# Performance work log

Hardware: AMD Instinct MI355X
Metric: run time of the kernel (lower is better)

Reference implementation:

```python
import jax, jax.numpy as jnp
import numpy as np

N_VERTICES = 2000
N_SENSORY = 784
N_EDGES = 500_000
BATCH = 32
T_STEPS = 5
LR_VALUES = 0.1


def setup_inputs() -> dict:
    key = jax.random.key(0)
    k1, k2, k3 = jax.random.split(key, 3)
    values = jax.random.normal(k1, (BATCH, N_VERTICES), dtype=jnp.float32)
    # weight_init 'normal 0.0' -> std = max(0.01, 0) = 0.01 in the torch module
    weights = jax.random.normal(k2, (N_EDGES,), dtype=jnp.float32) * 0.01
    edge_index = jax.random.randint(k3, (2, N_EDGES), 0, N_VERTICES, dtype=jnp.int32)
    # sensory nodes (first 784) are clamped; only internal nodes update
    update_mask = jnp.arange(N_VERTICES) >= N_SENSORY  # bool [N]
    return {
        "values": values,
        "weights": weights,
        "edge_index": edge_index,
        "update_mask": update_mask,
        "T": T_STEPS,
    }


def reference(values, weights, edge_index, update_mask, T):
    """Iterative predictive-coding message passing.

    Each step:
      pred_i  = sum_{e: dst(e)=i} w_e * f(values[src(e)])   (gather-mul-scatter)
      err     = values - pred
      back_j  = sum_{e: src(e)=j} w_e * err[dst(e)]          (reverse scatter)
      dv      = err - f'(values) * back                      (dE/dx)
      values  = values - lr * dv   (sensory nodes clamped)
    """
    src, dst = edge_index[0], edge_index[1]
    n = values.shape[1]
    mask = update_mask[None, :]

    def step(v, _):
        fx = jnp.tanh(v)                                   # [B, N]
        msg = weights[None, :] * fx[:, src]                # [B, E]
        pred = jax.ops.segment_sum(msg.T, dst, num_segments=n).T  # [B, N]
        err = v - pred                                     # [B, N]
        w_err = weights[None, :] * err[:, dst]             # [B, E]
        back = jax.ops.segment_sum(w_err.T, src, num_segments=n).T  # [B, N]
        fprime = 1.0 - fx * fx                             # tanh'
        dv = err - fprime * back
        v_new = jnp.where(mask, v - LR_VALUES * dv, v)
        return v_new, None

    v_final, _ = jax.lax.scan(step, values, None, length=T)
    return v_final
```

## Files before the change

### kernel.cpp

```cpp
#include <hip/hip_runtime.h>
#include <hip/hip_bf16.h>


#define N_V     2000
#define N_SENS  784
#define N_INT   (N_V - N_SENS)
#define N_E     500000
#define T_STEPS 5
#define LR_VAL  0.1f
#define NVB     (N_V * 32)
#define NVH     (N_V * 16)
#define KP      2016
#define NCH     63
#define NT1     125
#define NT2     76
#define FRAG_N  (2 * NCH * 64 * 8)
#define NBLK    250
#define EPB     2000

typedef float  f32x4 __attribute__((ext_vector_type(4)));
typedef short  s16x8 __attribute__((ext_vector_type(8)));

__device__ __forceinline__ float bits_to_f32(unsigned u) {
    union { unsigned u; float f; } c; c.u = u; return c.f;
}
__device__ __forceinline__ unsigned f32_to_bits(float f) {
    union { float f; unsigned u; } c; c.f = f; return c.u;
}
__device__ __forceinline__ unsigned short f32_to_bf16(float f) {
    unsigned u = f32_to_bits(f);
    return (unsigned short)((u + 0x7FFFu + ((u >> 16) & 1u)) >> 16);
}
__device__ __forceinline__ float bf16_to_f32(unsigned short s) {
    return bits_to_f32((unsigned)s << 16);
}

__device__ __forceinline__ int aposKB(int k, int b) {
    int c = k >> 5, q = (k >> 3) & 3, j = k & 7;
    int h = b >> 4, m = b & 15;
    return (((h * NCH + c) * 64) + q * 16 + m) * 8 + j;
}


__global__ void k_zero_u4(uint4* p, int n4) {
    uint4 z = {0u, 0u, 0u, 0u};
    for (int t = blockIdx.x * blockDim.x + threadIdx.x; t < n4; t += gridDim.x * blockDim.x)
        p[t] = z;
}

__global__ __launch_bounds__(256) void k_cnt(const int* __restrict__ dst,
                                             int* __restrict__ cnt_g) {
    __shared__ int cnt[NT1];
    int b = blockIdx.x;
    for (int i = threadIdx.x; i < NT1; i += 256) cnt[i] = 0;
    __syncthreads();
    int base = b * EPB;
    for (int e = base + threadIdx.x; e < base + EPB; e += 256)
        atomicAdd(&cnt[dst[e] >> 4], 1);
    __syncthreads();
    for (int t = threadIdx.x; t < NT1; t += 256)
        cnt_g[t * 256 + b] = cnt[t];
}

__global__ __launch_bounds__(256) void k_scan_a(const int* __restrict__ cnt_g,
                                                int* __restrict__ base_g,
                                                int* __restrict__ totals) {
    __shared__ int sh[256];
    int t = blockIdx.x, tid = threadIdx.x;
    int v = (tid < NBLK) ? cnt_g[t * 256 + tid] : 0;
    sh[tid] = v;
    __syncthreads();
    for (int off = 1; off < 256; off <<= 1) {
        int x = (tid >= off) ? sh[tid - off] : 0;
        __syncthreads();
        sh[tid] += x;
        __syncthreads();
    }
    if (tid < NBLK) base_g[t * 256 + tid] = sh[tid] - v;
    if (tid == 255) totals[t] = sh[255];
}

__global__ void k_scan_b(const int* __restrict__ totals, int* __restrict__ tile_start) {
    if (threadIdx.x == 0 && blockIdx.x == 0) {
        int acc = 0;
        for (int t = 0; t < NT1; ++t) { tile_start[t] = acc; acc += totals[t]; }
        tile_start[NT1] = acc;
    }
}

__global__ __launch_bounds__(256) void k_place(
        const int* __restrict__ src, const int* __restrict__ dst,
        const float* __restrict__ w, const int* __restrict__ base_g,
        const int* __restrict__ tile_start, unsigned* __restrict__ pk_g) {
    __shared__ int cur[NT1];
    int b = blockIdx.x;
    for (int t = threadIdx.x; t < NT1; t += 256)
        cur[t] = tile_start[t] + base_g[t * 256 + b];
    __syncthreads();
    int base = b * EPB;
    for (int e = base + threadIdx.x; e < base + EPB; e += 256) {
        int d = dst[e];
        int tb = d >> 4;
        unsigned pk = ((unsigned)f32_to_bf16(w[e]) << 16)
                    | ((unsigned)(d & 15) << 11) | (unsigned)src[e];
        int p = atomicAdd(&cur[tb], 1);
        pk_g[p] = pk;
    }
}

__global__ __launch_bounds__(256) void k_build(
        const unsigned* __restrict__ pk_g, const int* __restrict__ tile_start,
        uint4* __restrict__ WAbf4, unsigned short* __restrict__ WAd) {
    __shared__ float acc[8][KP];
    int tile = blockIdx.x >> 1, half = blockIdx.x & 1;
    for (int i = threadIdx.x; i < 8 * KP / 4; i += 256)
        ((float4*)&acc[0][0])[i] = make_float4(0.f, 0.f, 0.f, 0.f);
    __syncthreads();
    int beg = tile_start[tile], end = tile_start[tile + 1];
    for (int e = beg + threadIdx.x; e < end; e += 256) {
        unsigned pk = pk_g[e];
        int row = (int)((pk >> 11) & 15u);
        if ((row >> 3) == half)
            atomicAdd(&acc[row & 7][pk & 0x7FFu], bf16_to_f32((unsigned short)(pk >> 16)));
    }
    __syncthreads();
    for (int i = threadIdx.x; i < 8 * 252; i += 256) {
        int rr = i / 252, g = i - rr * 252;
        int c = g >> 2, q = g & 3;
        int col = g * 8;
        unsigned short r[8];
        #pragma unroll
        for (int j = 0; j < 8; ++j) r[j] = f32_to_bf16(acc[rr][col + j]);
        uint4 val = *(const uint4*)r;
        int m = half * 8 + rr;
        WAbf4[((tile * NCH + c) * 64) + q * 16 + m] = val;
        *(uint4*)(WAd + (size_t)(tile * 16 + m) * KP + col) = val;
    }
}

__global__ void k_trB(const unsigned short* __restrict__ WAd, uint4* __restrict__ WBf4) {
    int t = blockIdx.x * blockDim.x + threadIdx.x;
    if (t < NT2 * NCH * 64) {
        int tile = t / (NCH * 64);
        int rem = t - tile * (NCH * 64);
        int c = rem >> 6, l = rem & 63;
        int jcol = N_SENS + tile * 16 + (l & 15);
        int k0 = c * 32 + (l >> 4) * 8;
        unsigned short r[8];
        #pragma unroll
        for (int j = 0; j < 8; ++j)
            r[j] = (k0 + j < N_V) ? WAd[(size_t)(k0 + j) * KP + jcol] : (unsigned short)0;
        WBf4[t] = *(const uint4*)r;
    }
}

__global__ void k_init(const float* __restrict__ vin, float* __restrict__ v,
                       unsigned short* __restrict__ fxA) {
    int t = blockIdx.x * blockDim.x + threadIdx.x;
    if (t < NVB) {
        int i = t >> 5, b = t & 31;
        float x = vin[b * N_V + i];
        v[t] = x;
        fxA[aposKB(i, b)] = f32_to_bf16(tanhf(x));
    }
}

__global__ __launch_bounds__(256) void k_gemm1(
        const uint4* __restrict__ WAbf4, const uint4* __restrict__ fxA4,
        const float* __restrict__ v_cur, unsigned short* __restrict__ errA) {
    __shared__ float red[2304];
    int tile = blockIdx.x;
    int w = threadIdx.x >> 6, l = threadIdx.x & 63;
    int cbeg = w * 16, cend = (cbeg + 16 < NCH) ? cbeg + 16 : NCH;
    f32x4 acc0 = {0.f, 0.f, 0.f, 0.f}, acc1 = {0.f, 0.f, 0.f, 0.f};
    for (int c = cbeg; c < cend; ++c) {
        uint4 bfrag = WAbf4[(tile * NCH + c) * 64 + l];
        uint4 a0 = fxA4[c * 64 + l];
        uint4 a1 = fxA4[(NCH + c) * 64 + l];
        acc0 = __builtin_amdgcn_mfma_f32_16x16x32_bf16(*(s16x8*)&a0, *(s16x8*)&bfrag, acc0, 0, 0, 0);
        acc1 = __builtin_amdgcn_mfma_f32_16x16x32_bf16(*(s16x8*)&a1, *(s16x8*)&bfrag, acc1, 0, 0, 0);
    }
    float* my = &red[w * 576 + l * 9];
    #pragma unroll
    for (int r = 0; r < 4; ++r) { my[r] = acc0[r]; my[4 + r] = acc1[r]; }
    __syncthreads();
    if (w == 0) {
        float s[8];
        #pragma unroll
        for (int r = 0; r < 8; ++r)
            s[r] = red[l * 9 + r] + red[576 + l * 9 + r]
                 + red[1152 + l * 9 + r] + red[1728 + l * 9 + r];
        int i = tile * 16 + (l & 15);
        int q = l >> 4;
        int c2 = i >> 5, q2 = (i >> 3) & 3, j2 = i & 7;
        #pragma unroll
        for (int h = 0; h < 2; ++h) {
            const float4 v4 = *(const float4*)(v_cur + (i << 5) + h * 16 + q * 4);
            int base = ((h * NCH + c2) * 64 + q2 * 16) * 8 + j2;
            errA[base + (q * 4 + 0) * 8] = f32_to_bf16(v4.x - s[h * 4 + 0]);
            errA[base + (q * 4 + 1) * 8] = f32_to_bf16(v4.y - s[h * 4 + 1]);
            errA[base + (q * 4 + 2) * 8] = f32_to_bf16(v4.z - s[h * 4 + 2]);
            errA[base + (q * 4 + 3) * 8] = f32_to_bf16(v4.w - s[h * 4 + 3]);
        }
    }
}

__global__ __launch_bounds__(256) void k_gemm2(
        const uint4* __restrict__ WBf4, const uint4* __restrict__ errA4,
        unsigned short* __restrict__ errA, unsigned short* __restrict__ fxA,
        float* __restrict__ v_cur) {
    __shared__ float red[2304];
    int tile = blockIdx.x;
    int w = threadIdx.x >> 6, l = threadIdx.x & 63;
    int cbeg = w * 16, cend = (cbeg + 16 < NCH) ? cbeg + 16 : NCH;
    f32x4 acc0 = {0.f, 0.f, 0.f, 0.f}, acc1 = {0.f, 0.f, 0.f, 0.f};
    for (int c = cbeg; c < cend; ++c) {
        uint4 bfrag = WBf4[(tile * NCH + c) * 64 + l];
        uint4 a0 = errA4[c * 64 + l];
        uint4 a1 = errA4[(NCH + c) * 64 + l];
        acc0 = __builtin_amdgcn_mfma_f32_16x16x32_bf16(*(s16x8*)&a0, *(s16x8*)&bfrag, acc0, 0, 0, 0);
        acc1 = __builtin_amdgcn_mfma_f32_16x16x32_bf16(*(s16x8*)&a1, *(s16x8*)&bfrag, acc1, 0, 0, 0);
    }
    float* my = &red[w * 576 + l * 9];
    #pragma unroll
    for (int r = 0; r < 4; ++r) { my[r] = acc0[r]; my[4 + r] = acc1[r]; }
    __syncthreads();
    if (w == 0) {
        float s[8];
        #pragma unroll
        for (int r = 0; r < 8; ++r)
            s[r] = red[l * 9 + r] + red[576 + l * 9 + r]
                 + red[1152 + l * 9 + r] + red[1728 + l * 9 + r];
        int j = N_SENS + tile * 16 + (l & 15);
        int q = l >> 4;
        int c2 = j >> 5, q2 = (j >> 3) & 3, j2 = j & 7;
        #pragma unroll
        for (int h = 0; h < 2; ++h) {
            float4 v4 = *(const float4*)(v_cur + (j << 5) + h * 16 + q * 4);
            int base = ((h * NCH + c2) * 64 + q2 * 16) * 8 + j2;
            float vv[4] = {v4.x, v4.y, v4.z, v4.w};
            #pragma unroll
            for (int r = 0; r < 4; ++r) {
                float back = s[h * 4 + r];
                float e0 = bf16_to_f32(errA[base + (q * 4 + r) * 8]);
                float fxv = tanhf(vv[r]);
                float vn = vv[r] - LR_VAL * (e0 - (1.f - fxv * fxv) * back);
                vv[r] = vn;
                fxA[base + (q * 4 + r) * 8] = f32_to_bf16(tanhf(vn));
            }
            float4 o = {vv[0], vv[1], vv[2], vv[3]};
            *(float4*)(v_cur + (j << 5) + h * 16 + q * 4) = o;
        }
    }
}

__global__ void k_out(const float* __restrict__ v, float* __restrict__ out) {
    int t = blockIdx.x * blockDim.x + threadIdx.x;
    if (t < NVB) {
        int b = t / N_V;
        int i = t - b * N_V;
        out[t] = v[(i << 5) + b];
    }
}

__global__ void k_cast_in(const float* __restrict__ vin, float* __restrict__ v) {
    int t = blockIdx.x * blockDim.x + threadIdx.x;
    if (t < NVB) {
        int i = t >> 5, b = t & 31;
        v[t] = vin[b * N_V + i];
    }
}


__global__ void k_zero_i32(int* a, int n) {
    int t = blockIdx.x * blockDim.x + threadIdx.x;
    if (t < n) a[t] = 0;
}

__global__ void k_hist(const int* __restrict__ src, const int* __restrict__ dst,
                       int* cnt_dst, int* cnt_src) {
    int e = blockIdx.x * blockDim.x + threadIdx.x;
    if (e < N_E) {
        atomicAdd(&cnt_dst[dst[e]], 1);
        atomicAdd(&cnt_src[src[e]], 1);
    }
}

__global__ __launch_bounds__(1024) void k_scan(int* cnt_a, int* rp_a,
                                               int* cnt_b, int* rp_b) {
    __shared__ int sh[1024];
    int t = threadIdx.x;
    for (int pass = 0; pass < 2; ++pass) {
        int* cnt = pass ? cnt_b : cnt_a;
        int* rp  = pass ? rp_b  : rp_a;
        int i0 = 2 * t, i1 = 2 * t + 1;
        int c0 = (i0 < N_V) ? cnt[i0] : 0;
        int c1 = (i1 < N_V) ? cnt[i1] : 0;
        __syncthreads();
        sh[t] = c0 + c1;
        __syncthreads();
        for (int off = 1; off < 1024; off <<= 1) {
            int v = (t >= off) ? sh[t - off] : 0;
            __syncthreads();
            sh[t] += v;
            __syncthreads();
        }
        int incl = sh[t];
        int e0 = incl - (c0 + c1);
        int e1 = e0 + c0;
        if (i0 <= N_V) rp[i0] = e0;
        if (i1 <= N_V) rp[i1] = e1;
        if (i0 < N_V) cnt[i0] = e0;
        if (i1 < N_V) cnt[i1] = e1;
    }
}

__global__ void k_scatter(const int* __restrict__ src, const int* __restrict__ dst,
                          const float* __restrict__ w,
                          int* cur_dst, int* cur_src,
                          unsigned* __restrict__ pk_dst, unsigned* __restrict__ pk_src) {
    int e = blockIdx.x * blockDim.x + threadIdx.x;
    if (e < N_E) {
        int s = src[e], d = dst[e];
        unsigned wbits = (unsigned)f32_to_bf16(w[e]);
        int p = atomicAdd(&cur_dst[d], 1);
        pk_dst[p] = (wbits << 16) | (unsigned)s;
        int q = atomicAdd(&cur_src[s], 1);
        pk_src[q] = (wbits << 16) | (unsigned)d;
    }
}

__global__ void k_fx_csr(const float* __restrict__ v, unsigned short* __restrict__ fx) {
    int t = blockIdx.x * blockDim.x + threadIdx.x;
    if (t < NVB) {
        int i = t >> 5, b = t & 31;
        int h = b >> 4, b16 = b & 15;
        fx[h * NVH + i * 16 + b16] = f32_to_bf16(tanhf(v[t]));
    }
}

__global__ __launch_bounds__(256) void k_pred_err(
        const float* __restrict__ v, const unsigned short* __restrict__ fx,
        const int* __restrict__ rp, const unsigned* __restrict__ pk,
        unsigned short* __restrict__ err) {
    __shared__ unsigned short tab[NVH];
    int h  = blockIdx.x / 250;
    int vg = blockIdx.x % 250;
    {
        const uint4* g = (const uint4*)(fx + h * NVH);
        uint4* l = (uint4*)tab;
        for (int i = threadIdx.x; i < NVH / 8; i += 256) l[i] = g[i];
    }
    __syncthreads();
    int wave = threadIdx.x >> 6;
    int lane = threadIdx.x & 63;
    int b16 = lane & 15, epar = lane >> 4;
    for (int k = 0; k < 2; ++k) {
        int vid = vg * 8 + wave * 2 + k;
        int beg = rp[vid], end = rp[vid + 1];
        float sum = 0.f;
        for (int e = beg + epar; e < end; e += 4) {
            unsigned p = pk[e];
            float w = bits_to_f32(p & 0xFFFF0000u);
            int nb = (int)(p & 0xFFFFu);
            sum += w * bf16_to_f32(tab[nb * 16 + b16]);
        }
        sum += __shfl_xor(sum, 16, 64);
        sum += __shfl_xor(sum, 32, 64);
        if (epar == 0) {
            float vo = v[(vid << 5) + h * 16 + b16];
            err[h * NVH + vid * 16 + b16] = f32_to_bf16(vo - sum);
        }
    }
}

__global__ __launch_bounds__(256) void k_back_upd(
        const unsigned short* __restrict__ fx, const unsigned short* __restrict__ err,
        const int* __restrict__ rp, const unsigned* __restrict__ pk,
        float* __restrict__ v) {
    __shared__ unsigned short tab[NVH];
    int h  = blockIdx.x / 152;
    int vg = blockIdx.x % 152;
    {
        const uint4* g = (const uint4*)(err + h * NVH);
        uint4* l = (uint4*)tab;
        for (int i = threadIdx.x; i < NVH / 8; i += 256) l[i] = g[i];
    }
    __syncthreads();
    int wave = threadIdx.x >> 6;
    int lane = threadIdx.x & 63;
    int b16 = lane & 15, epar = lane >> 4;
    for (int k = 0; k < 2; ++k) {
        int vid = N_SENS + vg * 8 + wave * 2 + k;
        if (vid >= N_V) continue;
        int beg = rp[vid], end = rp[vid + 1];
        float sum = 0.f;
        for (int e = beg + epar; e < end; e += 4) {
            unsigned p = pk[e];
            float w = bits_to_f32(p & 0xFFFF0000u);
            int nb = (int)(p & 0xFFFFu);
            sum += w * bf16_to_f32(tab[nb * 16 + b16]);
        }
        sum += __shfl_xor(sum, 16, 64);
        sum += __shfl_xor(sum, 32, 64);
        if (epar == 0) {
            float e0  = bf16_to_f32(tab[vid * 16 + b16]);
            float fxv = bf16_to_f32(fx[h * NVH + vid * 16 + b16]);
            float dv = e0 - (1.f - fxv * fxv) * sum;
            v[(vid << 5) + h * 16 + b16] -= LR_VAL * dv;
        }
    }
}


extern "C" void kernel_launch(void* const* d_in, const int* in_sizes, int n_in,
                              void* d_out, int out_size, void* d_ws, size_t ws_size,
                              hipStream_t stream) {
    const float* vals = (const float*)d_in[0];
    const float* wts  = (const float*)d_in[1];
    const int* ei = (const int*)d_in[2];
    const int* src = ei;
    const int* dst = ei + N_E;
    float* out = (float*)d_out;

    const int EB = (N_E + 255) / 256;

    const size_t WABF_T = (size_t)NT1 * NCH * 64;
    const size_t WBF_T  = (size_t)NT2 * NCH * 64;
    const size_t WAD_N  = (size_t)N_V * KP;
    const size_t need = (size_t)N_E * 4 + 2 * NT1 * 256 * 4 + 512 * 4
                      + WAD_N * 2 + WABF_T * 16 + WBF_T * 16
                      + 2 * (size_t)FRAG_N * 2 + NVB * 4 + 256;

    if (ws_size >= need) {
        unsigned* pk_g = (unsigned*)d_ws;
        int* cnt_g  = (int*)(pk_g + N_E);
        int* base_g = cnt_g + NT1 * 256;
        int* totals = base_g + NT1 * 256;
        int* tile_start = totals + 128;
        unsigned short* WAd = (unsigned short*)(tile_start + 384);
        uint4* WAbf4 = (uint4*)(WAd + WAD_N);
        uint4* WBf4  = WAbf4 + WABF_T;
        unsigned short* fxA  = (unsigned short*)(WBf4 + WBF_T);
        unsigned short* errA = fxA + FRAG_N;
        float* v_cur = (float*)(errA + FRAG_N);

        k_zero_u4<<<64, 256, 0, stream>>>((uint4*)fxA, (int)(2 * (size_t)FRAG_N * 2 / 16));
        k_cnt<<<NBLK, 256, 0, stream>>>(dst, cnt_g);
        k_scan_a<<<NT1, 256, 0, stream>>>(cnt_g, base_g, totals);
        k_scan_b<<<1, 64, 0, stream>>>(totals, tile_start);
        k_place<<<NBLK, 256, 0, stream>>>(src, dst, wts, base_g, tile_start, pk_g);
        k_build<<<2 * NT1, 256, 0, stream>>>(pk_g, tile_start, WAbf4, WAd);
        k_trB<<<(int)((WBF_T + 255) / 256), 256, 0, stream>>>(WAd, WBf4);
        k_init<<<250, 256, 0, stream>>>(vals, v_cur, fxA);

        for (int t = 0; t < T_STEPS; ++t) {
            k_gemm1<<<NT1, 256, 0, stream>>>(WAbf4, (const uint4*)fxA, v_cur, errA);
            k_gemm2<<<NT2, 256, 0, stream>>>(WBf4, (const uint4*)errA, errA, fxA, v_cur);
        }
        k_out<<<250, 256, 0, stream>>>(v_cur, out);
    } else {
        float* v_cur = (float*)d_ws;
        unsigned short* fx_g  = (unsigned short*)(v_cur + NVB);
        unsigned short* err_g = fx_g + NVB;
        int* rp_dst  = (int*)(err_g + NVB);
        int* rp_src  = rp_dst + 2048;
        int* cur_dst = rp_src + 2048;
        int* cur_src = cur_dst + 2048;
        unsigned* pk_dst = (unsigned*)(cur_src + 2048);
        unsigned* pk_src = pk_dst + N_E;

        k_zero_i32<<<16, 256, 0, stream>>>(cur_dst, 4096);
        k_hist<<<EB, 256, 0, stream>>>(src, dst, cur_dst, cur_src);
        k_scan<<<1, 1024, 0, stream>>>(cur_dst, rp_dst, cur_src, rp_src);
        k_scatter<<<EB, 256, 0, stream>>>(src, dst, wts, cur_dst, cur_src,
                                          pk_dst, pk_src);
        k_cast_in<<<250, 256, 0, stream>>>(vals, v_cur);
        for (int t = 0; t < T_STEPS; ++t) {
            k_fx_csr<<<250, 256, 0, stream>>>(v_cur, fx_g);
            k_pred_err<<<500, 256, 0, stream>>>(v_cur, fx_g, rp_dst, pk_dst, err_g);
            k_back_upd<<<304, 256, 0, stream>>>(fx_g, err_g, rp_src, pk_src, v_cur);
        }
        k_out<<<250, 256, 0, stream>>>(v_cur, out);
    }
}
```

Before: 180.1 us.

## Fuse setup and time-step kernels into two cooperative persistent kernels

Replaces the chain of about eighteen small kernel launches (build passes, init, ten GEMM launches, output) with two cooperative kernels that use grid-wide syncs between phases. The step kernel also splits each GEMM tile across two blocks by batch half, so 250 blocks each run one MFMA chain instead of 125/76 blocks running two. Only the 16 padding rows of the fragment buffers are zeroed now, not the whole buffers. The aim is to cut launch gaps and raise occupancy, at the cost of grid.sync overhead and a dependence on all 250 blocks being co-resident.

New measurement: 612.8 us. 3.4x slower.

```diff
diff --git a/kernel.cpp b/kernel.cpp
--- a/kernel.cpp
+++ b/kernel.cpp
@@ -1,5 +1,6 @@
 #include <hip/hip_runtime.h>
 #include <hip/hip_bf16.h>
+#include <hip/hip_cooperative_groups.h>
 
 
 #define N_V     2000
@@ -18,6 +19,8 @@
 #define NBLK    250
 #define EPB     2000
 
+namespace cg = cooperative_groups;
+
 typedef float  f32x4 __attribute__((ext_vector_type(4)));
 typedef short  s16x8 __attribute__((ext_vector_type(8)));
 
@@ -42,232 +45,212 @@
 }
 
 
-__global__ void k_zero_u4(uint4* p, int n4) {
-    uint4 z = {0u, 0u, 0u, 0u};
-    for (int t = blockIdx.x * blockDim.x + threadIdx.x; t < n4; t += gridDim.x * blockDim.x)
-        p[t] = z;
-}
-
-__global__ __launch_bounds__(256) void k_cnt(const int* __restrict__ dst,
-                                             int* __restrict__ cnt_g) {
-    __shared__ int cnt[NT1];
-    int b = blockIdx.x;
-    for (int i = threadIdx.x; i < NT1; i += 256) cnt[i] = 0;
-    __syncthreads();
-    int base = b * EPB;
-    for (int e = base + threadIdx.x; e < base + EPB; e += 256)
-        atomicAdd(&cnt[dst[e] >> 4], 1);
-    __syncthreads();
-    for (int t = threadIdx.x; t < NT1; t += 256)
-        cnt_g[t * 256 + b] = cnt[t];
-}
-
-__global__ __launch_bounds__(256) void k_scan_a(const int* __restrict__ cnt_g,
-                                                int* __restrict__ base_g,
-                                                int* __restrict__ totals) {
-    __shared__ int sh[256];
-    int t = blockIdx.x, tid = threadIdx.x;
-    int v = (tid < NBLK) ? cnt_g[t * 256 + tid] : 0;
-    sh[tid] = v;
-    __syncthreads();
-    for (int off = 1; off < 256; off <<= 1) {
-        int x = (tid >= off) ? sh[tid - off] : 0;
-        __syncthreads();
-        sh[tid] += x;
-        __syncthreads();
-    }
-    if (tid < NBLK) base_g[t * 256 + tid] = sh[tid] - v;
-    if (tid == 255) totals[t] = sh[255];
-}
-
-__global__ void k_scan_b(const int* __restrict__ totals, int* __restrict__ tile_start) {
-    if (threadIdx.x == 0 && blockIdx.x == 0) {
-        int acc = 0;
-        for (int t = 0; t < NT1; ++t) { tile_start[t] = acc; acc += totals[t]; }
-        tile_start[NT1] = acc;
-    }
-}
-
-__global__ __launch_bounds__(256) void k_place(
+__global__ __launch_bounds__(256) void k_build_all(
         const int* __restrict__ src, const int* __restrict__ dst,
-        const float* __restrict__ w, const int* __restrict__ base_g,
-        const int* __restrict__ tile_start, unsigned* __restrict__ pk_g) {
-    __shared__ int cur[NT1];
-    int b = blockIdx.x;
-    for (int t = threadIdx.x; t < NT1; t += 256)
-        cur[t] = tile_start[t] + base_g[t * 256 + b];
-    __syncthreads();
-    int base = b * EPB;
-    for (int e = base + threadIdx.x; e < base + EPB; e += 256) {
-        int d = dst[e];
-        int tb = d >> 4;
-        unsigned pk = ((unsigned)f32_to_bf16(w[e]) << 16)
-                    | ((unsigned)(d & 15) << 11) | (unsigned)src[e];
-        int p = atomicAdd(&cur[tb], 1);
-        pk_g[p] = pk;
-    }
-}
-
-__global__ __launch_bounds__(256) void k_build(
-        const unsigned* __restrict__ pk_g, const int* __restrict__ tile_start,
-        uint4* __restrict__ WAbf4, unsigned short* __restrict__ WAd) {
+        const float* __restrict__ w, const float* __restrict__ vin,
+        int* cnt_g, int* base_g, int* totals, int* tile_start,
+        unsigned* pk_g, uint4* WAbf4, unsigned short* WAd, uint4* WBf4,
+        unsigned short* fxA, unsigned short* errA, float* v_cur) {
+    cg::grid_group grid = cg::this_grid();
     __shared__ float acc[8][KP];
-    int tile = blockIdx.x >> 1, half = blockIdx.x & 1;
-    for (int i = threadIdx.x; i < 8 * KP / 4; i += 256)
-        ((float4*)&acc[0][0])[i] = make_float4(0.f, 0.f, 0.f, 0.f);
-    __syncthreads();
-    int beg = tile_start[tile], end = tile_start[tile + 1];
-    for (int e = beg + threadIdx.x; e < end; e += 256) {
-        unsigned pk = pk_g[e];
-        int row = (int)((pk >> 11) & 15u);
-        if ((row >> 3) == half)
-            atomicAdd(&acc[row & 7][pk & 0x7FFu], bf16_to_f32((unsigned short)(pk >> 16)));
-    }
-    __syncthreads();
-    for (int i = threadIdx.x; i < 8 * 252; i += 256) {
-        int rr = i / 252, g = i - rr * 252;
-        int c = g >> 2, q = g & 3;
-        int col = g * 8;
-        unsigned short r[8];
-        #pragma unroll
-        for (int j = 0; j < 8; ++j) r[j] = f32_to_bf16(acc[rr][col + j]);
-        uint4 val = *(const uint4*)r;
-        int m = half * 8 + rr;
-        WAbf4[((tile * NCH + c) * 64) + q * 16 + m] = val;
-        *(uint4*)(WAd + (size_t)(tile * 16 + m) * KP + col) = val;
-    }
-}
-
-__global__ void k_trB(const unsigned short* __restrict__ WAd, uint4* __restrict__ WBf4) {
-    int t = blockIdx.x * blockDim.x + threadIdx.x;
-    if (t < NT2 * NCH * 64) {
-        int tile = t / (NCH * 64);
-        int rem = t - tile * (NCH * 64);
-        int c = rem >> 6, l = rem & 63;
-        int jcol = N_SENS + tile * 16 + (l & 15);
-        int k0 = c * 32 + (l >> 4) * 8;
-        unsigned short r[8];
-        #pragma unroll
-        for (int j = 0; j < 8; ++j)
-            r[j] = (k0 + j < N_V) ? WAd[(size_t)(k0 + j) * KP + jcol] : (unsigned short)0;
-        WBf4[t] = *(const uint4*)r;
-    }
-}
-
-__global__ void k_init(const float* __restrict__ vin, float* __restrict__ v,
-                       unsigned short* __restrict__ fxA) {
-    int t = blockIdx.x * blockDim.x + threadIdx.x;
-    if (t < NVB) {
-        int i = t >> 5, b = t & 31;
-        float x = vin[b * N_V + i];
-        v[t] = x;
-        fxA[aposKB(i, b)] = f32_to_bf16(tanhf(x));
-    }
-}
-
-__global__ __launch_bounds__(256) void k_gemm1(
-        const uint4* __restrict__ WAbf4, const uint4* __restrict__ fxA4,
-        const float* __restrict__ v_cur, unsigned short* __restrict__ errA) {
-    __shared__ float red[2304];
-    int tile = blockIdx.x;
-    int w = threadIdx.x >> 6, l = threadIdx.x & 63;
-    int cbeg = w * 16, cend = (cbeg + 16 < NCH) ? cbeg + 16 : NCH;
-    f32x4 acc0 = {0.f, 0.f, 0.f, 0.f}, acc1 = {0.f, 0.f, 0.f, 0.f};
-    for (int c = cbeg; c < cend; ++c) {
-        uint4 bfrag = WAbf4[(tile * NCH + c) * 64 + l];
-        uint4 a0 = fxA4[c * 64 + l];
-        uint4 a1 = fxA4[(NCH + c) * 64 + l];
-        acc0 = __builtin_amdgcn_mfma_f32_16x16x32_bf16(*(s16x8*)&a0, *(s16x8*)&bfrag, acc0, 0, 0, 0);
-        acc1 = __builtin_amdgcn_mfma_f32_16x16x32_bf16(*(s16x8*)&a1, *(s16x8*)&bfrag, acc1, 0, 0, 0);
-    }
-    float* my = &red[w * 576 + l * 9];
-    #pragma unroll
-    for (int r = 0; r < 4; ++r) { my[r] = acc0[r]; my[4 + r] = acc1[r]; }
-    __syncthreads();
-    if (w == 0) {
-        float s[8];
-        #pragma unroll
-        for (int r = 0; r < 8; ++r)
-            s[r] = red[l * 9 + r] + red[576 + l * 9 + r]
-                 + red[1152 + l * 9 + r] + red[1728 + l * 9 + r];
-        int i = tile * 16 + (l & 15);
-        int q = l >> 4;
-        int c2 = i >> 5, q2 = (i >> 3) & 3, j2 = i & 7;
-        #pragma unroll
-        for (int h = 0; h < 2; ++h) {
-            const float4 v4 = *(const float4*)(v_cur + (i << 5) + h * 16 + q * 4);
-            int base = ((h * NCH + c2) * 64 + q2 * 16) * 8 + j2;
-            errA[base + (q * 4 + 0) * 8] = f32_to_bf16(v4.x - s[h * 4 + 0]);
-            errA[base + (q * 4 + 1) * 8] = f32_to_bf16(v4.y - s[h * 4 + 1]);
-            errA[base + (q * 4 + 2) * 8] = f32_to_bf16(v4.z - s[h * 4 + 2]);
-            errA[base + (q * 4 + 3) * 8] = f32_to_bf16(v4.w - s[h * 4 + 3]);
-        }
-    }
-}
-
-__global__ __launch_bounds__(256) void k_gemm2(
-        const uint4* __restrict__ WBf4, const uint4* __restrict__ errA4,
-        unsigned short* __restrict__ errA, unsigned short* __restrict__ fxA,
-        float* __restrict__ v_cur) {
-    __shared__ float red[2304];
-    int tile = blockIdx.x;
-    int w = threadIdx.x >> 6, l = threadIdx.x & 63;
-    int cbeg = w * 16, cend = (cbeg + 16 < NCH) ? cbeg + 16 : NCH;
-    f32x4 acc0 = {0.f, 0.f, 0.f, 0.f}, acc1 = {0.f, 0.f, 0.f, 0.f};
-    for (int c = cbeg; c < cend; ++c) {
-        uint4 bfrag = WBf4[(tile * NCH + c) * 64 + l];
-        uint4 a0 = errA4[c * 64 + l];
-        uint4 a1 = errA4[(NCH + c) * 64 + l];
-        acc0 = __builtin_amdgcn_mfma_f32_16x16x32_bf16(*(s16x8*)&a0, *(s16x8*)&bfrag, acc0, 0, 0, 0);
-        acc1 = __builtin_amdgcn_mfma_f32_16x16x32_bf16(*(s16x8*)&a1, *(s16x8*)&bfrag, acc1, 0, 0, 0);
-    }
-    float* my = &red[w * 576 + l * 9];
-    #pragma unroll
-    for (int r = 0; r < 4; ++r) { my[r] = acc0[r]; my[4 + r] = acc1[r]; }
-    __syncthreads();
-    if (w == 0) {
-        float s[8];
-        #pragma unroll
-        for (int r = 0; r < 8; ++r)
-            s[r] = red[l * 9 + r] + red[576 + l * 9 + r]
-                 + red[1152 + l * 9 + r] + red[1728 + l * 9 + r];
-        int j = N_SENS + tile * 16 + (l & 15);
-        int q = l >> 4;
-        int c2 = j >> 5, q2 = (j >> 3) & 3, j2 = j & 7;
-        #pragma unroll
-        for (int h = 0; h < 2; ++h) {
-            float4 v4 = *(const float4*)(v_cur + (j << 5) + h * 16 + q * 4);
-            int base = ((h * NCH + c2) * 64 + q2 * 16) * 8 + j2;
-            float vv[4] = {v4.x, v4.y, v4.z, v4.w};
+    int bx = blockIdx.x, tid = threadIdx.x;
+
+    {
+        int t = bx * 256 + tid;
+        if (t < 16 * 32) {
+            int k = 2000 + (t >> 5), b = t & 31;
+            fxA[aposKB(k, b)] = 0;
+            errA[aposKB(k, b)] = 0;
+        }
+    }
+    {
+        int* cnt = (int*)&acc[0][0];
+        for (int i = tid; i < NT1; i += 256) cnt[i] = 0;
+        __syncthreads();
+        int base = bx * EPB;
+        for (int e = base + tid; e < base + EPB; e += 256)
+            atomicAdd(&cnt[dst[e] >> 4], 1);
+        __syncthreads();
+        for (int t = tid; t < NT1; t += 256) cnt_g[t * 256 + bx] = cnt[t];
+    }
+    grid.sync();
+    if (bx < NT1) {
+        int* sh = (int*)&acc[0][0];
+        int v = (tid < NBLK) ? cnt_g[bx * 256 + tid] : 0;
+        sh[tid] = v;
+        __syncthreads();
+        for (int off = 1; off < 256; off <<= 1) {
+            int x = (tid >= off) ? sh[tid - off] : 0;
+            __syncthreads();
+            sh[tid] += x;
+            __syncthreads();
+        }
+        if (tid < NBLK) base_g[bx * 256 + tid] = sh[tid] - v;
+        if (tid == 255) totals[bx] = sh[255];
+    }
+    grid.sync();
+    if (bx == 0 && tid == 0) {
+        int a = 0;
+        for (int t = 0; t < NT1; ++t) { tile_start[t] = a; a += totals[t]; }
+        tile_start[NT1] = a;
+    }
+    grid.sync();
+    {
+        int* cur = (int*)&acc[0][0];
+        for (int t = tid; t < NT1; t += 256)
+            cur[t] = tile_start[t] + base_g[t * 256 + bx];
+        __syncthreads();
+        int base = bx * EPB;
+        for (int e = base + tid; e < base + EPB; e += 256) {
+            int d = dst[e];
+            unsigned pk = ((unsigned)f32_to_bf16(w[e]) << 16)
+                        | ((unsigned)(d & 15) << 11) | (unsigned)src[e];
+            int p = atomicAdd(&cur[d >> 4], 1);
+            pk_g[p] = pk;
+        }
+    }
+    grid.sync();
+    {
+        int tile = bx >> 1, half = bx & 1;
+        for (int i = tid; i < 8 * KP / 4; i += 256)
+            ((float4*)&acc[0][0])[i] = make_float4(0.f, 0.f, 0.f, 0.f);
+        __syncthreads();
+        int beg = tile_start[tile], end = tile_start[tile + 1];
+        for (int e = beg + tid; e < end; e += 256) {
+            unsigned pk = pk_g[e];
+            int row = (int)((pk >> 11) & 15u);
+            if ((row >> 3) == half)
+                atomicAdd(&acc[row & 7][pk & 0x7FFu],
+                          bf16_to_f32((unsigned short)(pk >> 16)));
+        }
+        __syncthreads();
+        for (int i = tid; i < 8 * 252; i += 256) {
+            int rr = i / 252, gg = i - rr * 252;
+            int c = gg >> 2, q = gg & 3;
+            int col = gg * 8;
+            unsigned short r[8];
             #pragma unroll
-            for (int r = 0; r < 4; ++r) {
-                float back = s[h * 4 + r];
-                float e0 = bf16_to_f32(errA[base + (q * 4 + r) * 8]);
-                float fxv = tanhf(vv[r]);
-                float vn = vv[r] - LR_VAL * (e0 - (1.f - fxv * fxv) * back);
-                vv[r] = vn;
-                fxA[base + (q * 4 + r) * 8] = f32_to_bf16(tanhf(vn));
+            for (int j = 0; j < 8; ++j) r[j] = f32_to_bf16(acc[rr][col + j]);
+            uint4 val = *(const uint4*)r;
+            int m = half * 8 + rr;
+            WAbf4[((tile * NCH + c) * 64) + q * 16 + m] = val;
+            *(uint4*)(WAd + (size_t)(tile * 16 + m) * KP + col) = val;
+        }
+    }
+    grid.sync();
+    {
+        const int stride = NBLK * 256;
+        for (int t = bx * 256 + tid; t < NT2 * NCH * 64; t += stride) {
+            int tile = t / (NCH * 64);
+            int rem = t - tile * (NCH * 64);
+            int c = rem >> 6, l = rem & 63;
+            int jcol = N_SENS + tile * 16 + (l & 15);
+            int k0 = c * 32 + (l >> 4) * 8;
+            unsigned short r[8];
+            #pragma unroll
+            for (int j = 0; j < 8; ++j)
+                r[j] = (k0 + j < N_V) ? WAd[(size_t)(k0 + j) * KP + jcol]
+                                      : (unsigned short)0;
+            WBf4[t] = *(const uint4*)r;
+        }
+        for (int t = bx * 256 + tid; t < NVB; t += stride) {
+            int i = t >> 5, b = t & 31;
+            float x = vin[b * N_V + i];
+            v_cur[t] = x;
+            fxA[aposKB(i, b)] = f32_to_bf16(tanhf(x));
+        }
+    }
+}
+
+
+__global__ __launch_bounds__(256) void k_steps(
+        const uint4* __restrict__ WAbf4, const uint4* __restrict__ WBf4,
+        unsigned short* fxA, unsigned short* errA, float* v_cur,
+        float* __restrict__ out) {
+    cg::grid_group grid = cg::this_grid();
+    __shared__ float red[1300];
+    int bx = blockIdx.x, tid = threadIdx.x;
+    int w = tid >> 6, l = tid & 63;
+    const uint4* fxA4  = (const uint4*)fxA;
+    const uint4* errA4 = (const uint4*)errA;
+
+    for (int t = 0; t < T_STEPS; ++t) {
+        {
+            int tile = bx >> 1, h = bx & 1;
+            int cbeg = w * 16, cend = (cbeg + 16 < NCH) ? cbeg + 16 : NCH;
+            f32x4 acc = {0.f, 0.f, 0.f, 0.f};
+            for (int c = cbeg; c < cend; ++c) {
+                uint4 bfrag = WAbf4[(tile * NCH + c) * 64 + l];
+                uint4 a = fxA4[(h * NCH + c) * 64 + l];
+                acc = __builtin_amdgcn_mfma_f32_16x16x32_bf16(
+                          *(s16x8*)&a, *(s16x8*)&bfrag, acc, 0, 0, 0);
             }
-            float4 o = {vv[0], vv[1], vv[2], vv[3]};
-            *(float4*)(v_cur + (j << 5) + h * 16 + q * 4) = o;
-        }
-    }
-}
-
-__global__ void k_out(const float* __restrict__ v, float* __restrict__ out) {
-    int t = blockIdx.x * blockDim.x + threadIdx.x;
-    if (t < NVB) {
-        int b = t / N_V;
-        int i = t - b * N_V;
-        out[t] = v[(i << 5) + b];
-    }
-}
-
-__global__ void k_cast_in(const float* __restrict__ vin, float* __restrict__ v) {
-    int t = blockIdx.x * blockDim.x + threadIdx.x;
-    if (t < NVB) {
-        int i = t >> 5, b = t & 31;
-        v[t] = vin[b * N_V + i];
+            float* my = &red[w * 325 + l * 5];
+            #pragma unroll
+            for (int r = 0; r < 4; ++r) my[r] = acc[r];
+            __syncthreads();
+            if (w == 0) {
+                float s[4];
+                #pragma unroll
+                for (int r = 0; r < 4; ++r)
+                    s[r] = red[l * 5 + r] + red[325 + l * 5 + r]
+                         + red[650 + l * 5 + r] + red[975 + l * 5 + r];
+                int i = tile * 16 + (l & 15);
+                int q = l >> 4;
+                int c2 = i >> 5, q2 = (i >> 3) & 3, j2 = i & 7;
+                const float4 v4 = *(const float4*)(v_cur + (i << 5) + h * 16 + q * 4);
+                int base = ((h * NCH + c2) * 64 + q2 * 16) * 8 + j2;
+                errA[base + (q * 4 + 0) * 8] = f32_to_bf16(v4.x - s[0]);
+                errA[base + (q * 4 + 1) * 8] = f32_to_bf16(v4.y - s[1]);
+                errA[base + (q * 4 + 2) * 8] = f32_to_bf16(v4.z - s[2]);
+                errA[base + (q * 4 + 3) * 8] = f32_to_bf16(v4.w - s[3]);
+            }
+        }
+        grid.sync();
+        if (bx < 2 * NT2) {
+            int tile = bx >> 1, h = bx & 1;
+            int cbeg = w * 16, cend = (cbeg + 16 < NCH) ? cbeg + 16 : NCH;
+            f32x4 acc = {0.f, 0.f, 0.f, 0.f};
+            for (int c = cbeg; c < cend; ++c) {
+                uint4 bfrag = WBf4[(tile * NCH + c) * 64 + l];
+                uint4 a = errA4[(h * NCH + c) * 64 + l];
+                acc = __builtin_amdgcn_mfma_f32_16x16x32_bf16(
+                          *(s16x8*)&a, *(s16x8*)&bfrag, acc, 0, 0, 0);
+            }
+            float* my = &red[w * 325 + l * 5];
+            #pragma unroll
+            for (int r = 0; r < 4; ++r) my[r] = acc[r];
+            __syncthreads();
+            if (w == 0) {
+                float s[4];
+                #pragma unroll
+                for (int r = 0; r < 4; ++r)
+                    s[r] = red[l * 5 + r] + red[325 + l * 5 + r]
+                         + red[650 + l * 5 + r] + red[975 + l * 5 + r];
+                int j = N_SENS + tile * 16 + (l & 15);
+                int q = l >> 4;
+                int c2 = j >> 5, q2 = (j >> 3) & 3, j2 = j & 7;
+                float4 v4 = *(const float4*)(v_cur + (j << 5) + h * 16 + q * 4);
+                int base = ((h * NCH + c2) * 64 + q2 * 16) * 8 + j2;
+                float vv[4] = {v4.x, v4.y, v4.z, v4.w};
+                #pragma unroll
+                for (int r = 0; r < 4; ++r) {
+                    float e0 = bf16_to_f32(errA[base + (q * 4 + r) * 8]);
+                    float fxv = tanhf(vv[r]);
+                    float vn = vv[r] - LR_VAL * (e0 - (1.f - fxv * fxv) * s[r]);
+                    vv[r] = vn;
+                    fxA[base + (q * 4 + r) * 8] = f32_to_bf16(tanhf(vn));
+                }
+                float4 o = {vv[0], vv[1], vv[2], vv[3]};
+                *(float4*)(v_cur + (j << 5) + h * 16 + q * 4) = o;
+            }
+        }
+        grid.sync();
+    }
+    for (int t2 = bx * 256 + tid; t2 < NVB; t2 += NBLK * 256) {
+        int b = t2 / N_V;
+        int i = t2 - b * N_V;
+        out[t2] = v_cur[(i << 5) + b];
     }
 }
 
@@ -327,6 +310,14 @@
         pk_dst[p] = (wbits << 16) | (unsigned)s;
         int q = atomicAdd(&cur_src[s], 1);
         pk_src[q] = (wbits << 16) | (unsigned)d;
+    }
+}
+
+__global__ void k_cast_in(const float* __restrict__ vin, float* __restrict__ v) {
+    int t = blockIdx.x * blockDim.x + threadIdx.x;
+    if (t < NVB) {
+        int i = t >> 5, b = t & 31;
+        v[t] = vin[b * N_V + i];
     }
 }
 
@@ -412,6 +403,15 @@
     }
 }
 
+__global__ void k_out_fb(const float* __restrict__ v, float* __restrict__ out) {
+    int t = blockIdx.x * blockDim.x + threadIdx.x;
+    if (t < NVB) {
+        int b = t / N_V;
+        int i = t - b * N_V;
+        out[t] = v[(i << 5) + b];
+    }
+}
+
 
 extern "C" void kernel_launch(void* const* d_in, const int* in_sizes, int n_in,
                               void* d_out, int out_size, void* d_ws, size_t ws_size,
@@ -445,20 +445,18 @@
         unsigned short* errA = fxA + FRAG_N;
         float* v_cur = (float*)(errA + FRAG_N);
 
-        k_zero_u4<<<64, 256, 0, stream>>>((uint4*)fxA, (int)(2 * (size_t)FRAG_N * 2 / 16));
-        k_cnt<<<NBLK, 256, 0, stream>>>(dst, cnt_g);
-        k_scan_a<<<NT1, 256, 0, stream>>>(cnt_g, base_g, totals);
-        k_scan_b<<<1, 64, 0, stream>>>(totals, tile_start);
-        k_place<<<NBLK, 256, 0, stream>>>(src, dst, wts, base_g, tile_start, pk_g);
-        k_build<<<2 * NT1, 256, 0, stream>>>(pk_g, tile_start, WAbf4, WAd);
-        k_trB<<<(int)((WBF_T + 255) / 256), 256, 0, stream>>>(WAd, WBf4);
-        k_init<<<250, 256, 0, stream>>>(vals, v_cur, fxA);
-
-        for (int t = 0; t < T_STEPS; ++t) {
-            k_gemm1<<<NT1, 256, 0, stream>>>(WAbf4, (const uint4*)fxA, v_cur, errA);
-            k_gemm2<<<NT2, 256, 0, stream>>>(WBf4, (const uint4*)errA, errA, fxA, v_cur);
-        }
-        k_out<<<250, 256, 0, stream>>>(v_cur, out);
+        void* argsA[] = {(void*)&src, (void*)&dst, (void*)&wts, (void*)&vals,
+                         (void*)&cnt_g, (void*)&base_g, (void*)&totals,
+                         (void*)&tile_start, (void*)&pk_g, (void*)&WAbf4,
+                         (void*)&WAd, (void*)&WBf4, (void*)&fxA, (void*)&errA,
+                         (void*)&v_cur};
+        hipLaunchCooperativeKernel((const void*)k_build_all, dim3(NBLK), dim3(256),
+                                   argsA, 0, stream);
+
+        void* argsB[] = {(void*)&WAbf4, (void*)&WBf4, (void*)&fxA, (void*)&errA,
+                         (void*)&v_cur, (void*)&out};
+        hipLaunchCooperativeKernel((const void*)k_steps, dim3(NBLK), dim3(256),
+                                   argsB, 0, stream);
     } else {
         float* v_cur = (float*)d_ws;
         unsigned short* fx_g  = (unsigned short*)(v_cur + NVB);
@@ -481,6 +479,6 @@
             k_pred_err<<<500, 256, 0, stream>>>(v_cur, fx_g, rp_dst, pk_dst, err_g);
             k_back_upd<<<304, 256, 0, stream>>>(fx_g, err_g, rp_src, pk_src, v_cur);
         }
-        k_out<<<250, 256, 0, stream>>>(v_cur, out);
-    }
-}
+        k_out_fb<<<250, 256, 0, stream>>>(v_cur, out);
+    }
+}
```

## Split GEMM blocks across batch halves and fold zeroing and output into other kernels

Applied to the files above, without the earlier changes.

Each GEMM kernel now launches twice as many blocks, one per 16-wide batch half, so every block does a single MFMA chain and shared-memory reduction shrinks. The separate zero kernel is dropped: only the padding rows 2000-2015 of the fragment buffers are zeroed, inside k_cnt. The final output transpose kernel is removed. Sensory rows are written in k_init and internal rows in the last gemm2 step. The goal is better CU occupancy on the latency-bound GEMM loop and fewer kernel launches, at the cost of reading the weight fragments twice.

After: 172.0 us (median of 2 runs). -4.5%, faster.

```diff
diff --git a/kernel.cpp b/kernel.cpp
--- a/kernel.cpp
+++ b/kernel.cpp
@@ -42,16 +42,20 @@
 }
 
 
-__global__ void k_zero_u4(uint4* p, int n4) {
-    uint4 z = {0u, 0u, 0u, 0u};
-    for (int t = blockIdx.x * blockDim.x + threadIdx.x; t < n4; t += gridDim.x * blockDim.x)
-        p[t] = z;
-}
-
 __global__ __launch_bounds__(256) void k_cnt(const int* __restrict__ dst,
-                                             int* __restrict__ cnt_g) {
+                                             int* __restrict__ cnt_g,
+                                             unsigned short* __restrict__ fxA,
+                                             unsigned short* __restrict__ errA) {
     __shared__ int cnt[NT1];
     int b = blockIdx.x;
+    {
+        int t = b * 256 + threadIdx.x;
+        if (t < 16 * 32) {
+            int k = 2000 + (t >> 5), bb = t & 31;
+            fxA[aposKB(k, bb)] = 0;
+            errA[aposKB(k, bb)] = 0;
+        }
+    }
     for (int i = threadIdx.x; i < NT1; i += 256) cnt[i] = 0;
     __syncthreads();
     int base = b * EPB;
@@ -100,10 +104,9 @@
     int base = b * EPB;
     for (int e = base + threadIdx.x; e < base + EPB; e += 256) {
         int d = dst[e];
-        int tb = d >> 4;
         unsigned pk = ((unsigned)f32_to_bf16(w[e]) << 16)
                     | ((unsigned)(d & 15) << 11) | (unsigned)src[e];
-        int p = atomicAdd(&cur[tb], 1);
+        int p = atomicAdd(&cur[d >> 4], 1);
         pk_g[p] = pk;
     }
 }
@@ -155,119 +158,114 @@
 }
 
 __global__ void k_init(const float* __restrict__ vin, float* __restrict__ v,
-                       unsigned short* __restrict__ fxA) {
+                       unsigned short* __restrict__ fxA, float* __restrict__ out) {
     int t = blockIdx.x * blockDim.x + threadIdx.x;
     if (t < NVB) {
-        int i = t >> 5, b = t & 31;
-        float x = vin[b * N_V + i];
-        v[t] = x;
+        float x = vin[t];
+        int b = t / N_V;
+        int i = t - b * N_V;
+        v[(i << 5) + b] = x;
         fxA[aposKB(i, b)] = f32_to_bf16(tanhf(x));
+        if (i < N_SENS) out[t] = x;
     }
 }
 
 __global__ __launch_bounds__(256) void k_gemm1(
         const uint4* __restrict__ WAbf4, const uint4* __restrict__ fxA4,
         const float* __restrict__ v_cur, unsigned short* __restrict__ errA) {
-    __shared__ float red[2304];
-    int tile = blockIdx.x;
-    int w = threadIdx.x >> 6, l = threadIdx.x & 63;
-    int cbeg = w * 16, cend = (cbeg + 16 < NCH) ? cbeg + 16 : NCH;
-    f32x4 acc0 = {0.f, 0.f, 0.f, 0.f}, acc1 = {0.f, 0.f, 0.f, 0.f};
-    for (int c = cbeg; c < cend; ++c) {
-        uint4 bfrag = WAbf4[(tile * NCH + c) * 64 + l];
-        uint4 a0 = fxA4[c * 64 + l];
-        uint4 a1 = fxA4[(NCH + c) * 64 + l];
-        acc0 = __builtin_amdgcn_mfma_f32_16x16x32_bf16(*(s16x8*)&a0, *(s16x8*)&bfrag, acc0, 0, 0, 0);
-        acc1 = __builtin_amdgcn_mfma_f32_16x16x32_bf16(*(s16x8*)&a1, *(s16x8*)&bfrag, acc1, 0, 0, 0);
-    }
-    float* my = &red[w * 576 + l * 9];
+    __shared__ float red[1300];
+    int bx = blockIdx.x, tid = threadIdx.x;
+    int w = tid >> 6, l = tid & 63;
+    int tile = bx >> 1, h = bx & 1;
+    int cbeg = w * 16;
+    const uint4* bp = WAbf4 + (size_t)tile * NCH * 64 + cbeg * 64 + l;
+    const uint4* ap = fxA4 + (size_t)h * NCH * 64 + cbeg * 64 + l;
+    f32x4 acc = {0.f, 0.f, 0.f, 0.f};
     #pragma unroll
-    for (int r = 0; r < 4; ++r) { my[r] = acc0[r]; my[4 + r] = acc1[r]; }
+    for (int cc = 0; cc < 16; ++cc) {
+        if (cbeg + cc < NCH) {
+            uint4 bfrag = bp[cc * 64];
+            uint4 a = ap[cc * 64];
+            acc = __builtin_amdgcn_mfma_f32_16x16x32_bf16(
+                      *(s16x8*)&a, *(s16x8*)&bfrag, acc, 0, 0, 0);
+        }
+    }
+    float* my = &red[w * 325 + l * 5];
+    #pragma unroll
+    for (int r = 0; r < 4; ++r) my[r] = acc[r];
     __syncthreads();
     if (w == 0) {
-        float s[8];
+        float s[4];
         #pragma unroll
-        for (int r = 0; r < 8; ++r)
-            s[r] = red[l * 9 + r] + red[576 + l * 9 + r]
-                 + red[1152 + l * 9 + r] + red[1728 + l * 9 + r];
+        for (int r = 0; r < 4; ++r)
+            s[r] = red[l * 5 + r] + red[325 + l * 5 + r]
+                 + red[650 + l * 5 + r] + red[975 + l * 5 + r];
         int i = tile * 16 + (l & 15);
         int q = l >> 4;
         int c2 = i >> 5, q2 = (i >> 3) & 3, j2 = i & 7;
-        #pragma unroll
-        for (int h = 0; h < 2; ++h) {
-            const float4 v4 = *(const float4*)(v_cur + (i << 5) + h * 16 + q * 4);
-            int base = ((h * NCH + c2) * 64 + q2 * 16) * 8 + j2;
-            errA[base + (q * 4 + 0) * 8] = f32_to_bf16(v4.x - s[h * 4 + 0]);
-            errA[base + (q * 4 + 1) * 8] = f32_to_bf16(v4.y - s[h * 4 + 1]);
-            errA[base + (q * 4 + 2) * 8] = f32_to_bf16(v4.z - s[h * 4 + 2]);
-            errA[base + (q * 4 + 3) * 8] = f32_to_bf16(v4.w - s[h * 4 + 3]);
-        }
+        const float4 v4 = *(const float4*)(v_cur + (i << 5) + h * 16 + q * 4);
+        int base = ((h * NCH + c2) * 64 + q2 * 16) * 8 + j2;
+        errA[base + (q * 4 + 0) * 8] = f32_to_bf16(v4.x - s[0]);
+        errA[base + (q * 4 + 1) * 8] = f32_to_bf16(v4.y - s[1]);
+        errA[base + (q * 4 + 2) * 8] = f32_to_bf16(v4.z - s[2]);
+        errA[base + (q * 4 + 3) * 8] = f32_to_bf16(v4.w - s[3]);
     }
 }
 
 __global__ __launch_bounds__(256) void k_gemm2(
         const uint4* __restrict__ WBf4, const uint4* __restrict__ errA4,
         unsigned short* __restrict__ errA, unsigned short* __restrict__ fxA,
-        float* __restrict__ v_cur) {
-    __shared__ float red[2304];
-    int tile = blockIdx.x;
-    int w = threadIdx.x >> 6, l = threadIdx.x & 63;
-    int cbeg = w * 16, cend = (cbeg + 16 < NCH) ? cbeg + 16 : NCH;
-    f32x4 acc0 = {0.f, 0.f, 0.f, 0.f}, acc1 = {0.f, 0.f, 0.f, 0.f};
-    for (int c = cbeg; c < cend; ++c) {
-        uint4 bfrag = WBf4[(tile * NCH + c) * 64 + l];
-        uint4 a0 = errA4[c * 64 + l];
-        uint4 a1 = errA4[(NCH + c) * 64 + l];
-        acc0 = __builtin_amdgcn_mfma_f32_16x16x32_bf16(*(s16x8*)&a0, *(s16x8*)&bfrag, acc0, 0, 0, 0);
-        acc1 = __builtin_amdgcn_mfma_f32_16x16x32_bf16(*(s16x8*)&a1, *(s16x8*)&bfrag, acc1, 0, 0, 0);
-    }
-    float* my = &red[w * 576 + l * 9];
+        float* __restrict__ v_cur, float* __restrict__ out, int final_step) {
+    __shared__ float red[1300];
+    int bx = blockIdx.x, tid = threadIdx.x;
+    int w = tid >> 6, l = tid & 63;
+    int tile = bx >> 1, h = bx & 1;
+    int cbeg = w * 16;
+    const uint4* bp = WBf4 + (size_t)tile * NCH * 64 + cbeg * 64 + l;
+    const uint4* ap = errA4 + (size_t)h * NCH * 64 + cbeg * 64 + l;
+    f32x4 acc = {0.f, 0.f, 0.f, 0.f};
     #pragma unroll
-    for (int r = 0; r < 4; ++r) { my[r] = acc0[r]; my[4 + r] = acc1[r]; }
+    for (int cc = 0; cc < 16; ++cc) {
+        if (cbeg + cc < NCH) {
+            uint4 bfrag = bp[cc * 64];
+            uint4 a = ap[cc * 64];
+            acc = __builtin_amdgcn_mfma_f32_16x16x32_bf16(
+                      *(s16x8*)&a, *(s16x8*)&bfrag, acc, 0, 0, 0);
+        }
+    }
+    float* my = &red[w * 325 + l * 5];
+    #pragma unroll
+    for (int r = 0; r < 4; ++r) my[r] = acc[r];
     __syncthreads();
     if (w == 0) {
-        float s[8];
+        float s[4];
         #pragma unroll
-        for (int r = 0; r < 8; ++r)
-            s[r] = red[l * 9 + r] + red[576 + l * 9 + r]
-                 + red[1152 + l * 9 + r] + red[1728 + l * 9 + r];
+        for (int r = 0; r < 4; ++r)
+            s[r] = red[l * 5 + r] + red[325 + l * 5 + r]
+                 + red[650 + l * 5 + r] + red[975 + l * 5 + r];
         int j = N_SENS + tile * 16 + (l & 15);
         int q = l >> 4;
         int c2 = j >> 5, q2 = (j >> 3) & 3, j2 = j & 7;
+        float4 v4 = *(const float4*)(v_cur + (j << 5) + h * 16 + q * 4);
+        int base = ((h * NCH + c2) * 64 + q2 * 16) * 8 + j2;
+        float vv[4] = {v4.x, v4.y, v4.z, v4.w};
         #pragma unroll
-        for (int h = 0; h < 2; ++h) {
-            float4 v4 = *(const float4*)(v_cur + (j << 5) + h * 16 + q * 4);
-            int base = ((h * NCH + c2) * 64 + q2 * 16) * 8 + j2;
-            float vv[4] = {v4.x, v4.y, v4.z, v4.w};
+        for (int r = 0; r < 4; ++r) {
+            float e0 = bf16_to_f32(errA[base + (q * 4 + r) * 8]);
+            float fxv = tanhf(vv[r]);
+            float vn = vv[r] - LR_VAL * (e0 - (1.f - fxv * fxv) * s[r]);
+            vv[r] = vn;
+            fxA[base + (q * 4 + r) * 8] = f32_to_bf16(tanhf(vn));
+        }
+        float4 o = {vv[0], vv[1], vv[2], vv[3]};
+        *(float4*)(v_cur + (j << 5) + h * 16 + q * 4) = o;
+        if (final_step) {
             #pragma unroll
             for (int r = 0; r < 4; ++r) {
-                float back = s[h * 4 + r];
-                float e0 = bf16_to_f32(errA[base + (q * 4 + r) * 8]);
-                float fxv = tanhf(vv[r]);
-                float vn = vv[r] - LR_VAL * (e0 - (1.f - fxv * fxv) * back);
-                vv[r] = vn;
-                fxA[base + (q * 4 + r) * 8] = f32_to_bf16(tanhf(vn));
+                int b = h * 16 + q * 4 + r;
+                out[b * N_V + j] = vv[r];
             }
-            float4 o = {vv[0], vv[1], vv[2], vv[3]};
-            *(float4*)(v_cur + (j << 5) + h * 16 + q * 4) = o;
-        }
-    }
-}
-
-__global__ void k_out(const float* __restrict__ v, float* __restrict__ out) {
-    int t = blockIdx.x * blockDim.x + threadIdx.x;
-    if (t < NVB) {
-        int b = t / N_V;
-        int i = t - b * N_V;
-        out[t] = v[(i << 5) + b];
-    }
-}
-
-__global__ void k_cast_in(const float* __restrict__ vin, float* __restrict__ v) {
-    int t = blockIdx.x * blockDim.x + threadIdx.x;
-    if (t < NVB) {
-        int i = t >> 5, b = t & 31;
-        v[t] = vin[b * N_V + i];
+        }
     }
 }
 
@@ -330,6 +328,14 @@
     }
 }
 
+__global__ void k_cast_in(const float* __restrict__ vin, float* __restrict__ v) {
+    int t = blockIdx.x * blockDim.x + threadIdx.x;
+    if (t < NVB) {
+        int i = t >> 5, b = t & 31;
+        v[t] = vin[b * N_V + i];
+    }
+}
+
 __global__ void k_fx_csr(const float* __restrict__ v, unsigned short* __restrict__ fx) {
     int t = blockIdx.x * blockDim.x + threadIdx.x;
     if (t < NVB) {
@@ -412,6 +418,15 @@
     }
 }
 
+__global__ void k_out_fb(const float* __restrict__ v, float* __restrict__ out) {
+    int t = blockIdx.x * blockDim.x + threadIdx.x;
+    if (t < NVB) {
+        int b = t / N_V;
+        int i = t - b * N_V;
+        out[t] = v[(i << 5) + b];
+    }
+}
+
 
 extern "C" void kernel_launch(void* const* d_in, const int* in_sizes, int n_in,
                               void* d_out, int out_size, void* d_ws, size_t ws_size,
@@ -445,20 +460,19 @@
         unsigned short* errA = fxA + FRAG_N;
         float* v_cur = (float*)(errA + FRAG_N);
 
-        k_zero_u4<<<64, 256, 0, stream>>>((uint4*)fxA, (int)(2 * (size_t)FRAG_N * 2 / 16));
-        k_cnt<<<NBLK, 256, 0, stream>>>(dst, cnt_g);
+        k_cnt<<<NBLK, 256, 0, stream>>>(dst, cnt_g, fxA, errA);
         k_scan_a<<<NT1, 256, 0, stream>>>(cnt_g, base_g, totals);
         k_scan_b<<<1, 64, 0, stream>>>(totals, tile_start);
         k_place<<<NBLK, 256, 0, stream>>>(src, dst, wts, base_g, tile_start, pk_g);
         k_build<<<2 * NT1, 256, 0, stream>>>(pk_g, tile_start, WAbf4, WAd);
         k_trB<<<(int)((WBF_T + 255) / 256), 256, 0, stream>>>(WAd, WBf4);
-        k_init<<<250, 256, 0, stream>>>(vals, v_cur, fxA);
+        k_init<<<250, 256, 0, stream>>>(vals, v_cur, fxA, out);
 
         for (int t = 0; t < T_STEPS; ++t) {
-            k_gemm1<<<NT1, 256, 0, stream>>>(WAbf4, (const uint4*)fxA, v_cur, errA);
-            k_gemm2<<<NT2, 256, 0, stream>>>(WBf4, (const uint4*)errA, errA, fxA, v_cur);
-        }
-        k_out<<<250, 256, 0, stream>>>(v_cur, out);
+            k_gemm1<<<250, 256, 0, stream>>>(WAbf4, (const uint4*)fxA, v_cur, errA);
+            k_gemm2<<<152, 256, 0, stream>>>(WBf4, (const uint4*)errA, errA, fxA,
+                                             v_cur, out, (t == T_STEPS - 1) ? 1 : 0);
+        }
     } else {
         float* v_cur = (float*)d_ws;
         unsigned short* fx_g  = (unsigned short*)(v_cur + NVB);
@@ -481,6 +495,6 @@
             k_pred_err<<<500, 256, 0, stream>>>(v_cur, fx_g, rp_dst, pk_dst, err_g);
             k_back_upd<<<304, 256, 0, stream>>>(fx_g, err_g, rp_src, pk_src, v_cur);
         }
-        k_out<<<250, 256, 0, stream>>>(v_cur, out);
-    }
-}
+        k_out_fb<<<250, 256, 0, stream>>>(v_cur, out);
+    }
+}
```
